# Kernel tuning notes

Measured on AMD Instinct MI355X. Metric: run time of the kernel, lower is better.

The kernel has to match this reference:

```python
import jax, jax.numpy as jnp
import numpy as np

N_NODES = 50000
N_EDGES = 400000
IN_F, HID_F, OUT_F = 768, 16, 21


def setup_inputs() -> dict:
    key = jax.random.key(0)
    ks = jax.random.split(key, 7)
    feature = jax.random.normal(ks[0], (N_NODES, IN_F), dtype=jnp.float32)
    W1 = jax.random.normal(ks[1], (IN_F, HID_F), dtype=jnp.float32) * 0.03
    b1 = jax.random.normal(ks[2], (HID_F,), dtype=jnp.float32) * 0.01
    W2 = jax.random.normal(ks[3], (HID_F, OUT_F), dtype=jnp.float32) * 0.1
    b2 = jax.random.normal(ks[4], (OUT_F,), dtype=jnp.float32) * 0.01
    src = jax.random.randint(ks[5], (N_EDGES,), 0, N_NODES, dtype=jnp.int32)
    dst = jax.random.randint(ks[6], (N_EDGES,), 0, N_NODES, dtype=jnp.int32)
    return {"feature": feature, "W1": W1, "b1": b1, "W2": W2, "b2": b2,
            "src": src, "dst": dst}


def _gcn_agg(h, src, dst):
    # copy_src + sum reduce: gather source features along edges, scatter-add to dst
    return jax.ops.segment_sum(h[src], dst, num_segments=N_NODES)


def reference(feature, W1, b1, W2, b2, src, dst):
    # layer 1: aggregate then linear + relu
    h = _gcn_agg(feature, src, dst)            # [N, 768]
    h = jax.nn.relu(h @ W1 + b1)               # [N, 16]
    # layer 2: aggregate then linear (no activation)
    h = _gcn_agg(h, src, dst)                  # [N, 16]
    return h @ W2 + b2                         # [N, 21]
```

## Files before the change

kernel.cpp:

```cpp
#include <hip/hip_runtime.h>

#define NN 50000
#define NE 400000
#define INF 768
#define HF 16
#define OF 21
#define ELLW 40

#define FMA4(ACC, SS, VV) { (ACC).x += (SS)*(VV).x; (ACC).y += (SS)*(VV).y; \
                            (ACC).z += (SS)*(VV).z; (ACC).w += (SS)*(VV).w; }

__global__ __launch_bounds__(256) void scatter_kernel(const int* __restrict__ src,
                                                      const int* __restrict__ dst,
                                                      int* __restrict__ cnt,
                                                      int* __restrict__ ell) {
    int e = blockIdx.x * 256 + threadIdx.x;
    if (e >= NE) return;
    int d = dst[e];
    int pos = atomicAdd(&cnt[d], 1);
    if (pos < ELLW) ell[d * ELLW + pos] = src[e];
}

__device__ __forceinline__ void gload_lds16(const float* g, float* l) {
    __builtin_amdgcn_global_load_lds(
        (const __attribute__((address_space(1))) unsigned int*)g,
        (__attribute__((address_space(3))) unsigned int*)l,
        16, 0, 0);
}

__global__ __launch_bounds__(512, 2) void gemm1_kernel(const float* __restrict__ F,
                                                       const float* __restrict__ W1,
                                                       float* __restrict__ P) {
    __shared__ float Ws[INF * HF];
    __shared__ float Fb[2][64 * 64];

    const int tid = threadIdx.x;
    for (int i = tid; i < (INF * HF) / 4; i += 512) {
        const int k = i >> 2, jq = i & 3;
        const int dg = (k & 3) * 768 + (k >> 6) * 64 + (((k >> 4) & 3) << 4)
                     + (((k >> 2) & 3) << 2) + jq;
        *(float4*)(Ws + dg * 4) = *(const float4*)(W1 + i * 4);
    }

    const int wv = tid >> 6, lane = tid & 63;
    const int jq = lane & 3;
    const int koff = lane & 60;
    const int rowbase = blockIdx.x * 64;

    const int colb = (lane & 15) * 4;
    int srow0 = rowbase + wv * 8 + 0 + (lane >> 4);
    int srow1 = rowbase + wv * 8 + 4 + (lane >> 4);
    if (srow0 > NN - 1) srow0 = NN - 1;
    if (srow1 > NN - 1) srow1 = NN - 1;
    const float* sp0 = F + (size_t)srow0 * INF + colb;
    const float* sp1 = F + (size_t)srow1 * INF + colb;
    float* ld0a = &Fb[0][wv * 512];        float* ld0b = &Fb[0][wv * 512 + 256];
    float* ld1a = &Fb[1][wv * 512];        float* ld1b = &Fb[1][wv * 512 + 256];

    gload_lds16(sp0, ld0a);
    gload_lds16(sp1, ld0b);

    const float* lw = Ws + lane * 4;

    float4 acc[8];
#pragma unroll
    for (int r = 0; r < 8; ++r) acc[r] = make_float4(0.f, 0.f, 0.f, 0.f);

    __syncthreads();

#pragma unroll 1
    for (int t = 0; t < 12; ++t) {
        if (t < 11) {
            const int c = (t + 1) * 64;
            if ((t & 1) == 0) { gload_lds16(sp0 + c, ld1a); gload_lds16(sp1 + c, ld1b); }
            else              { gload_lds16(sp0 + c, ld0a); gload_lds16(sp1 + c, ld0b); }
        }
        const float* lwt = lw + t * 256;
        const float4 w0 = *(const float4*)(lwt + 0 * 3072);
        const float4 w1 = *(const float4*)(lwt + 1 * 3072);
        const float4 w2 = *(const float4*)(lwt + 2 * 3072);
        const float4 w3 = *(const float4*)(lwt + 3 * 3072);
        const float* fb = &Fb[t & 1][koff];
#pragma unroll
        for (int r = 0; r < 8; ++r) {
            const float4 f = *(const float4*)(fb + (wv * 8 + r) * 64);
            FMA4(acc[r], f.x, w0);
            FMA4(acc[r], f.y, w1);
            FMA4(acc[r], f.z, w2);
            FMA4(acc[r], f.w, w3);
        }
        __syncthreads();
    }

#pragma unroll
    for (int r = 0; r < 8; ++r) {
        float4 v = acc[r];
#define RED(X) { v.X += __shfl_xor(v.X, 4);  v.X += __shfl_xor(v.X, 8); \
                 v.X += __shfl_xor(v.X, 16); v.X += __shfl_xor(v.X, 32); }
        RED(x) RED(y) RED(z) RED(w)
#undef RED
        const int row = rowbase + wv * 8 + r;
        if (lane < 4 && row < NN)
            *(float4*)(P + (size_t)row * HF + jq * 4) = v;
    }
}

__global__ __launch_bounds__(256) void agg1_kernel(const float* __restrict__ P,
                                                   const int* __restrict__ cnt,
                                                   const int* __restrict__ ell,
                                                   float* __restrict__ A1) {
    int g = blockIdx.x * 256 + threadIdx.x;
    int node = g >> 4;
    if (node >= NN) return;
    const int l = g & 15, es = l >> 2, q = l & 3;
    int c = cnt[node]; if (c > ELLW) c = ELLW;
    const int* ep = ell + node * ELLW;

    float4 v = {0,0,0,0};
    for (int i = es; i < c; i += 4) {
        int s = ep[i];
        float4 p = *(const float4*)(P + (size_t)s * HF + q * 4);
        v.x += p.x; v.y += p.y; v.z += p.z; v.w += p.w;
    }
#define BFLY2(VAL) { VAL += __shfl_xor(VAL, 4); VAL += __shfl_xor(VAL, 8); }
    BFLY2(v.x) BFLY2(v.y) BFLY2(v.z) BFLY2(v.w)
#undef BFLY2
    if (es == 0)
        *(float4*)(A1 + (size_t)node * HF + q * 4) = v;
}

__global__ __launch_bounds__(256) void agg2out_kernel(const float* __restrict__ A1,
                                                      const float* __restrict__ b1,
                                                      const int* __restrict__ cnt,
                                                      const int* __restrict__ ell,
                                                      const float* __restrict__ W2,
                                                      const float* __restrict__ b2,
                                                      float* __restrict__ out) {
    __shared__ float W2s[HF * OF];
    __shared__ float b2s[OF];
    const int t = threadIdx.x;
    for (int i = t; i < HF * OF; i += 256) W2s[i] = W2[i];
    if (t < OF) b2s[t] = b2[t];
    __syncthreads();

    int g = blockIdx.x * 256 + t;
    int node = g >> 4;
    if (node >= NN) return;
    const int l = g & 15, es = l >> 2, q = l & 3;

    const float4 bb = *(const float4*)(b1 + q * 4);
    int c = cnt[node]; if (c > ELLW) c = ELLW;
    const int* ep = ell + node * ELLW;

    float4 v = {0,0,0,0};
    for (int i = es; i < c; i += 4) {
        int s = ep[i];
        float4 h = *(const float4*)(A1 + (size_t)s * HF + q * 4);
        h.x = fmaxf(h.x + bb.x, 0.0f);
        h.y = fmaxf(h.y + bb.y, 0.0f);
        h.z = fmaxf(h.z + bb.z, 0.0f);
        h.w = fmaxf(h.w + bb.w, 0.0f);
        v.x += h.x; v.y += h.y; v.z += h.z; v.w += h.w;
    }
#define BFLY2(VAL) { VAL += __shfl_xor(VAL, 4); VAL += __shfl_xor(VAL, 8); }
    BFLY2(v.x) BFLY2(v.y) BFLY2(v.z) BFLY2(v.w)
#undef BFLY2

    const float* w0 = W2s + (q * 4 + 0) * OF;
    const float* w1 = W2s + (q * 4 + 1) * OF;
    const float* w2 = W2s + (q * 4 + 2) * OF;
    const float* w3 = W2s + (q * 4 + 3) * OF;
    float o[OF];
#pragma unroll
    for (int cc = 0; cc < OF; ++cc)
        o[cc] = v.x * w0[cc] + v.y * w1[cc] + v.z * w2[cc] + v.w * w3[cc];
#pragma unroll
    for (int cc = 0; cc < OF; ++cc) {
        o[cc] += __shfl_xor(o[cc], 1);
        o[cc] += __shfl_xor(o[cc], 2);
    }
    if (es == 0) {
        float* op = out + (size_t)node * OF;
        for (int cc = q; cc < OF; cc += 4) op[cc] = o[cc] + b2s[cc];
    }
}

extern "C" void kernel_launch(void* const* d_in, const int* in_sizes, int n_in,
                              void* d_out, int out_size, void* d_ws, size_t ws_size,
                              hipStream_t stream) {
    const float* F   = (const float*)d_in[0];
    const float* W1  = (const float*)d_in[1];
    const float* b1  = (const float*)d_in[2];
    const float* W2  = (const float*)d_in[3];
    const float* b2  = (const float*)d_in[4];
    const int*   src = (const int*)d_in[5];
    const int*   dst = (const int*)d_in[6];
    float* out = (float*)d_out;

    char* ws = (char*)d_ws;
    int*   cnt = (int*)(ws);
    int*   ell = (int*)(ws + 200192);
    float* P   = (float*)(ws + 8200192);
    float* A1  = (float*)(ws + 11400192);

    (void)hipMemsetAsync(cnt, 0, NN * sizeof(int), stream);
    scatter_kernel<<<(NE + 255) / 256, 256, 0, stream>>>(src, dst, cnt, ell);
    gemm1_kernel<<<(NN + 63) / 64, 512, 0, stream>>>(F, W1, P);
    agg1_kernel<<<(NN * 16 + 255) / 256, 256, 0, stream>>>(P, cnt, ell, A1);
    agg2out_kernel<<<(NN * 16 + 255) / 256, 256, 0, stream>>>(A1, b1, cnt, ell, W2, b2, out);
}
```

Baseline: 300.6 us.

## Use per-wave 4-stage LDS ring with vmcnt waits instead of block barriers in gemm1

Restructures the feature-streaming GEMM so each wave owns a private 4-slot LDS ring, prefetches three tiles ahead, and waits with s_waitcnt vmcnt instead of __syncthreads each iteration. Blocks shrink to 256 threads covering 32 rows, so more blocks are launched. The goal is deeper memory-level parallelism and no block-wide barriers on this bandwidth-bound stage. It relies on vmcnt counting the LDS-direct loads correctly, and each block still reloads the 48KB W1 tile into LDS, which now happens twice as often in total.

```diff
diff --git a/kernel.cpp b/kernel.cpp
--- a/kernel.cpp
+++ b/kernel.cpp
@@ -28,14 +28,16 @@
         16, 0, 0);
 }
 
-__global__ __launch_bounds__(512, 2) void gemm1_kernel(const float* __restrict__ F,
+#define WAITV(N) asm volatile("s_waitcnt vmcnt(" #N ")" ::: "memory")
+
+__global__ __launch_bounds__(256, 2) void gemm1_kernel(const float* __restrict__ F,
                                                        const float* __restrict__ W1,
                                                        float* __restrict__ P) {
     __shared__ float Ws[INF * HF];
-    __shared__ float Fb[2][64 * 64];
+    __shared__ float Fs[4 * 4 * 512];
 
     const int tid = threadIdx.x;
-    for (int i = tid; i < (INF * HF) / 4; i += 512) {
+    for (int i = tid; i < (INF * HF) / 4; i += 256) {
         const int k = i >> 2, jq = i & 3;
         const int dg = (k & 3) * 768 + (k >> 6) * 64 + (((k >> 4) & 3) << 4)
                      + (((k >> 2) & 3) << 2) + jq;
@@ -45,20 +47,15 @@
     const int wv = tid >> 6, lane = tid & 63;
     const int jq = lane & 3;
     const int koff = lane & 60;
-    const int rowbase = blockIdx.x * 64;
-
-    const int colb = (lane & 15) * 4;
-    int srow0 = rowbase + wv * 8 + 0 + (lane >> 4);
-    int srow1 = rowbase + wv * 8 + 4 + (lane >> 4);
+    const int rowbase = blockIdx.x * 32 + wv * 8;
+
+    int srow0 = rowbase + 0 + (lane >> 4);
+    int srow1 = rowbase + 4 + (lane >> 4);
     if (srow0 > NN - 1) srow0 = NN - 1;
     if (srow1 > NN - 1) srow1 = NN - 1;
-    const float* sp0 = F + (size_t)srow0 * INF + colb;
-    const float* sp1 = F + (size_t)srow1 * INF + colb;
-    float* ld0a = &Fb[0][wv * 512];        float* ld0b = &Fb[0][wv * 512 + 256];
-    float* ld1a = &Fb[1][wv * 512];        float* ld1b = &Fb[1][wv * 512 + 256];
-
-    gload_lds16(sp0, ld0a);
-    gload_lds16(sp1, ld0b);
+    const float* sp0 = F + (size_t)srow0 * INF + (lane & 15) * 4;
+    const float* sp1 = F + (size_t)srow1 * INF + (lane & 15) * 4;
+    float* ring = Fs + wv * 2048;
 
     const float* lw = Ws + lane * 4;
 
@@ -68,29 +65,39 @@
 
     __syncthreads();
 
+#define STAGE(T, S) { gload_lds16(sp0 + (T) * 64, ring + (S) * 512); \
+                      gload_lds16(sp1 + (T) * 64, ring + (S) * 512 + 256); }
+
+#define COMPUTE(T, S) { \
+    const float* lwt = lw + (T) * 256; \
+    const float4 w0 = *(const float4*)(lwt + 0 * 3072); \
+    const float4 w1 = *(const float4*)(lwt + 1 * 3072); \
+    const float4 w2 = *(const float4*)(lwt + 2 * 3072); \
+    const float4 w3 = *(const float4*)(lwt + 3 * 3072); \
+    const float* fb = ring + (S) * 512 + koff; \
+    _Pragma("unroll") \
+    for (int r = 0; r < 8; ++r) { \
+        const float4 f = *(const float4*)(fb + r * 64); \
+        FMA4(acc[r], f.x, w0); \
+        FMA4(acc[r], f.y, w1); \
+        FMA4(acc[r], f.z, w2); \
+        FMA4(acc[r], f.w, w3); \
+    } }
+
+    STAGE(0, 0); STAGE(1, 1); STAGE(2, 2);
+
 #pragma unroll 1
-    for (int t = 0; t < 12; ++t) {
-        if (t < 11) {
-            const int c = (t + 1) * 64;
-            if ((t & 1) == 0) { gload_lds16(sp0 + c, ld1a); gload_lds16(sp1 + c, ld1b); }
-            else              { gload_lds16(sp0 + c, ld0a); gload_lds16(sp1 + c, ld0b); }
-        }
-        const float* lwt = lw + t * 256;
-        const float4 w0 = *(const float4*)(lwt + 0 * 3072);
-        const float4 w1 = *(const float4*)(lwt + 1 * 3072);
-        const float4 w2 = *(const float4*)(lwt + 2 * 3072);
-        const float4 w3 = *(const float4*)(lwt + 3 * 3072);
-        const float* fb = &Fb[t & 1][koff];
-#pragma unroll
-        for (int r = 0; r < 8; ++r) {
-            const float4 f = *(const float4*)(fb + (wv * 8 + r) * 64);
-            FMA4(acc[r], f.x, w0);
-            FMA4(acc[r], f.y, w1);
-            FMA4(acc[r], f.z, w2);
-            FMA4(acc[r], f.w, w3);
-        }
-        __syncthreads();
-    }
+    for (int t = 0; t < 9; ++t) {
+        STAGE(t + 3, (t + 3) & 3);
+        WAITV(6);
+        COMPUTE(t, t & 3);
+    }
+    WAITV(4); COMPUTE(9, 1);
+    WAITV(2); COMPUTE(10, 2);
+    WAITV(0); COMPUTE(11, 3);
+
+#undef STAGE
+#undef COMPUTE
 
 #pragma unroll
     for (int r = 0; r < 8; ++r) {
@@ -99,7 +106,7 @@
                  v.X += __shfl_xor(v.X, 16); v.X += __shfl_xor(v.X, 32); }
         RED(x) RED(y) RED(z) RED(w)
 #undef RED
-        const int row = rowbase + wv * 8 + r;
+        const int row = rowbase + r;
         if (lane < 4 && row < NN)
             *(float4*)(P + (size_t)row * HF + jq * 4) = v;
     }
@@ -205,7 +212,7 @@
 
     (void)hipMemsetAsync(cnt, 0, NN * sizeof(int), stream);
     scatter_kernel<<<(NE + 255) / 256, 256, 0, stream>>>(src, dst, cnt, ell);
-    gemm1_kernel<<<(NN + 63) / 64, 512, 0, stream>>>(F, W1, P);
+    gemm1_kernel<<<(NN + 31) / 32, 256, 0, stream>>>(F, W1, P);
     agg1_kernel<<<(NN * 16 + 255) / 256, 256, 0, stream>>>(P, cnt, ell, A1);
     agg2out_kernel<<<(NN * 16 + 255) / 256, 256, 0, stream>>>(A1, b1, cnt, ell, W2, b2, out);
 }
```

Result: slower. 309.8 us (+3.0%).
